# Kernel tuning notes

Hardware: AMD Instinct MI355X
Metric: run time of the kernel (lower is better)

Reference implementation:

```python
import jax, jax.numpy as jnp
import numpy as np

B, NS, NN = 1024, 1, 64
F = 128            # feat_dim = edge_dim = time_dim = pos_dim
DM = 4 * F         # model_dim = 512
H, DK = 2, 256     # n_head, d_k = d_v = model_dim // n_head
LN_EPS = 1e-5


def setup_inputs() -> dict:
    key = jax.random.key(0)
    ks = jax.random.split(key, 20)
    s = 0.02
    inp = {
        'src':   jax.random.normal(ks[0], (B, NS, F), jnp.float32),
        'src_t': jax.random.normal(ks[1], (B, NS, F), jnp.float32),
        'src_p': jax.random.normal(ks[2], (B, NS, F), jnp.float32),
        'seq':   jax.random.normal(ks[3], (B, NN, F), jnp.float32),
        'seq_t': jax.random.normal(ks[4], (B, NN, F), jnp.float32),
        'seq_e': jax.random.normal(ks[5], (B, NN, F), jnp.float32),
        'seq_p': jax.random.normal(ks[6], (B, NN, F), jnp.float32),
        'mask':  jax.random.randint(ks[7], (B, NS, NN), 0, 2).astype(bool),
        # MapBasedMultiHeadAttention params
        'wq': jax.random.normal(ks[8], (H * DK, DM), jnp.float32) * s,
        'wk': jax.random.normal(ks[9], (H * DK, DM), jnp.float32) * s,
        'wv': jax.random.normal(ks[10], (H * DK, DM), jnp.float32) * s,
        'wm': jax.random.normal(ks[11], (2 * DK,), jnp.float32) * s,   # weight_map: Linear(2*d_k, 1, bias=False)
        'fc_w': jax.random.normal(ks[12], (DM, H * DK), jnp.float32) * s,
        'fc_b': jnp.zeros((DM,), jnp.float32),
        'ln_g': jnp.ones((DM,), jnp.float32),
        'ln_b': jnp.zeros((DM,), jnp.float32),
        # MergeLayer(model_dim, feat_dim, feat_dim, feat_dim)
        'm1_w': jax.random.normal(ks[13], (F, DM + F), jnp.float32) * s,
        'm1_b': jnp.zeros((F,), jnp.float32),
        'm2_w': jax.random.normal(ks[14], (F, F), jnp.float32) * s,
        'm2_b': jnp.zeros((F,), jnp.float32),
    }
    return inp


def reference(src, src_t, src_p, seq, seq_t, seq_e, seq_p, mask,
              wq, wk, wv, wm, fc_w, fc_b, ln_g, ln_b, m1_w, m1_b, m2_w, m2_b):
    b, ns, f = src.shape
    nn = seq.shape[1]
    src_e = jnp.zeros((b, ns, f), src.dtype)  # edge feats of sources are zero
    q = jnp.concatenate([src, src_e, src_t, src_p], axis=-1)   # [B,NS,DM]
    k = jnp.concatenate([seq, seq_e, seq_t, seq_p], axis=-1)   # [B,NN,DM]

    # per-head projections: weight [H*DK, DM] -> [H, DK, DM]
    qh = jnp.einsum('bsd,hed->bshe', q, wq.reshape(H, DK, DM))  # [B,NS,H,DK]
    kh = jnp.einsum('bnd,hed->bnhe', k, wk.reshape(H, DK, DM))  # [B,NN,H,DK]
    vh = jnp.einsum('bnd,hed->bnhe', k, wv.reshape(H, DK, DM))  # [B,NN,H,DK]

    # weight_map(Linear over concat([q,k])) == q @ wm[:DK] + k @ wm[DK:]
    score_q = jnp.einsum('bshe,e->bhs', qh, wm[:DK])            # [B,H,NS]
    score_k = jnp.einsum('bnhe,e->bhn', kh, wm[DK:])            # [B,H,NN]
    attn = score_q[..., None] + score_k[:, :, None, :]          # [B,H,NS,NN]
    attn = jnp.where(mask[:, None, :, :], jnp.float32(-1e10), attn)
    attn = jax.nn.softmax(attn, axis=-1)

    out = jnp.einsum('bhsn,bnhe->bshe', attn, vh).reshape(b, ns, H * DK)
    out = jnp.einsum('bsd,ed->bse', out, fc_w) + fc_b           # fc
    out = jnp.where(out >= 0, out, 0.2 * out)                   # LeakyReLU(0.2)
    out = out + q                                               # residual
    mu = out.mean(axis=-1, keepdims=True)
    var = out.var(axis=-1, keepdims=True)
    out = (out - mu) / jnp.sqrt(var + LN_EPS) * ln_g + ln_b     # LayerNorm

    # MergeLayer (non_linear=True)
    x = jnp.concatenate([out, src], axis=-1)                    # [B,NS,DM+F]
    hdn = jax.nn.relu(jnp.einsum('bsd,ed->bse', x, m1_w) + m1_b)
    z = jnp.einsum('bsd,ed->bse', hdn, m2_w) + m2_b             # [B,NS,F]

    # attn in original layout: [n_head*B, len_q, len_k]
    attn_flat = attn.transpose(1, 0, 2, 3).reshape(H * b, ns, nn)
    return (z, attn_flat)
```

## Files before the change

kernel.cpp:

```cpp
#include <hip/hip_runtime.h>
#include <hip/hip_bf16.h>
#include <stdint.h>

#define B_   1024
#define NN_  64
#define F_   128
#define DM_  512
#define DK_  256

typedef unsigned short u16;
using f32x4  = __attribute__((ext_vector_type(4))) float;
using bf16x8 = __attribute__((ext_vector_type(8))) short;

__device__ __forceinline__ uint32_t f2bf(float x) {
  uint32_t u = __builtin_bit_cast(uint32_t, x);
  return (u + 0x7fffu + ((u >> 16) & 1u)) >> 16;
}
__device__ __forceinline__ float bf2f(uint32_t us) {
  return __builtin_bit_cast(float, us << 16);
}
__device__ __forceinline__ void split_pack(float x, float y, uint32_t& hp, uint32_t& lp) {
  uint32_t hx = f2bf(x), hy = f2bf(y);
  uint32_t lx = f2bf(x - bf2f(hx)), ly = f2bf(y - bf2f(hy));
  hp = hx | (hy << 16);
  lp = lx | (ly << 16);
}
__device__ __forceinline__ void split1(float x, u16& h, u16& l) {
  uint32_t hx = f2bf(x);
  h = (u16)hx;
  l = (u16)f2bf(x - bf2f(hx));
}
template <int CTRL>
__device__ __forceinline__ float dppadd(float x) {
  int r = __builtin_amdgcn_mov_dpp(__builtin_bit_cast(int, x), CTRL, 0xF, 0xF, true);
  return x + __builtin_bit_cast(float, r);
}
__device__ __forceinline__ float red16(float p) {
  p = dppadd<0xB1>(p);
  p = dppadd<0x4E>(p);
  p = dppadd<0x114>(p);
  p = dppadd<0x118>(p);
  return p;
}

__global__ __launch_bounds__(256) void k_prep(
    const float* __restrict__ wv, const float* __restrict__ fc_w,
    const float* __restrict__ m1_w, const float* __restrict__ m2_w,
    const float* __restrict__ wk, const float* __restrict__ wm,
    u16* __restrict__ fc_hi, u16* __restrict__ fc_lo,
    u16* __restrict__ wvT_hi, u16* __restrict__ wvT_lo,
    u16* __restrict__ m1_hi, u16* __restrict__ m1_lo,
    u16* __restrict__ m2_hi, u16* __restrict__ m2_lo,
    float* __restrict__ wkc) {
  __shared__ float tile[32][33];
  int tid = threadIdx.x;
  int bx = blockIdx.x;

  if (bx >= 256) {
    int t = bx - 256;
    int h = t >> 3, dc = t & 7;
    int w = tid >> 6, l = tid & 63;
    int d = dc * 64 + l;
    const float* base = wk + (size_t)(h * DK_ + w * 64) * DM_ + d;
    float sacc[8] = {0.f, 0.f, 0.f, 0.f, 0.f, 0.f, 0.f, 0.f};
    #pragma unroll
    for (int e = 0; e < 64; ++e)
      sacc[e & 7] += base[e * DM_] * wm[DK_ + w * 64 + e];
    float s = ((sacc[0] + sacc[1]) + (sacc[2] + sacc[3])) +
              ((sacc[4] + sacc[5]) + (sacc[6] + sacc[7]));
    float* part = &tile[0][0];
    part[w * 64 + l] = s;
    __syncthreads();
    if (w == 0)
      wkc[h * DM_ + d] = part[l] + part[64 + l] + part[128 + l] + part[192 + l];
    return;
  }

  int gtid = bx * 256 + tid;
  int nthr = 256 * 256;
  for (int i = gtid; i < DM_ * DM_; i += nthr) split1(fc_w[i], fc_hi[i], fc_lo[i]);
  for (int i = gtid; i < F_ * (DM_ + F_); i += nthr) split1(m1_w[i], m1_hi[i], m1_lo[i]);
  for (int i = gtid; i < F_ * F_; i += nthr) split1(m2_w[i], m2_hi[i], m2_lo[i]);

  int e0 = (bx >> 4) * 32, d0 = (bx & 15) * 32;
  int rr = tid >> 3, c4 = (tid & 7) * 4;
  float4 v = *(const float4*)(wv + (e0 + rr) * DM_ + d0 + c4);
  tile[rr][c4] = v.x; tile[rr][c4 + 1] = v.y;
  tile[rr][c4 + 2] = v.z; tile[rr][c4 + 3] = v.w;
  __syncthreads();
  int dr = tid >> 3, ec = (tid & 7) * 4;
  #pragma unroll
  for (int q = 0; q < 4; ++q) {
    int idx = (d0 + dr) * DM_ + e0 + ec + q;
    split1(tile[ec + q][dr], wvT_hi[idx], wvT_lo[idx]);
  }
}

__device__ __forceinline__ f32x4 mfma_tile_split(
    const u16* __restrict__ Ahi, const u16* __restrict__ Alo, int lda,
    const u16* __restrict__ Bhi, const u16* __restrict__ Blo, int ldb, int K) {
  int l = threadIdx.x & 63;
  int r = l & 15, g = l >> 4;
  int offA = r * lda + g * 8;
  int offB = r * ldb + g * 8;
  f32x4 acc = {0.f, 0.f, 0.f, 0.f};
  for (int k = 0; k < K; k += 32) {
    bf16x8 ah = *(const bf16x8*)(Ahi + offA + k);
    bf16x8 al = *(const bf16x8*)(Alo + offA + k);
    bf16x8 bh = *(const bf16x8*)(Bhi + offB + k);
    bf16x8 bl = *(const bf16x8*)(Blo + offB + k);
    acc = __builtin_amdgcn_mfma_f32_16x16x32_bf16(ah, bh, acc, 0, 0, 0);
    acc = __builtin_amdgcn_mfma_f32_16x16x32_bf16(ah, bl, acc, 0, 0, 0);
    acc = __builtin_amdgcn_mfma_f32_16x16x32_bf16(al, bh, acc, 0, 0, 0);
  }
  return acc;
}

__global__ __launch_bounds__(256) void k_wcomb(
    const u16* __restrict__ fc_hi, const u16* __restrict__ fc_lo,
    const u16* __restrict__ wvT_hi, const u16* __restrict__ wvT_lo,
    u16* __restrict__ wc_hi, u16* __restrict__ wc_lo) {
  int wid = threadIdx.x >> 6;
  int n0g = blockIdx.y * 32;
  int h = n0g >> 9, d0 = n0g & 511;
  int m0 = blockIdx.x * 32 + (wid >> 1) * 16;
  int nb = d0 + (wid & 1) * 16;
  f32x4 acc = mfma_tile_split(fc_hi + m0 * DM_ + h * DK_,
                              fc_lo + m0 * DM_ + h * DK_, DM_,
                              wvT_hi + nb * DM_ + h * DK_,
                              wvT_lo + nb * DM_ + h * DK_, DM_, DK_);
  int l = threadIdx.x & 63, r = l & 15, g = l >> 4;
  #pragma unroll
  for (int i = 0; i < 4; ++i) {
    int m = m0 + g * 4 + i;
    int idx = m * 1024 + n0g + (wid & 1) * 16 + r;
    split1(acc[i], wc_hi[idx], wc_lo[idx]);
  }
}

__global__ __launch_bounds__(256) void k_score(
    const float* __restrict__ seq, const float* __restrict__ seq_e,
    const float* __restrict__ seq_t, const float* __restrict__ seq_p,
    const float* __restrict__ wkc, float* __restrict__ S_part) {
  int b = blockIdx.x, w = blockIdx.y;
  int tid = threadIdx.x;
  int ww = tid >> 6, l = tid & 63;
  int r16 = l >> 4, c16 = l & 15;
  const float* arr = (w == 0 ? seq : (w == 1 ? seq_e : (w == 2 ? seq_t : seq_p)));
  int cb = 8 * c16;
  float c0[8], c1[8];
  #pragma unroll
  for (int u = 0; u < 8; ++u) {
    c0[u] = wkc[w * 128 + cb + u];
    c1[u] = wkc[512 + w * 128 + cb + u];
  }
  const float* base = arr + (size_t)b * 8192 + (size_t)(ww * 16 + r16) * 128 + cb;
  size_t s0i = (((size_t)w * 1024 + b) * 2 + 0) * 64;
  size_t s1i = (((size_t)w * 1024 + b) * 2 + 1) * 64;

  float4 va[4], vb[4];
  #pragma unroll
  for (int i = 0; i < 4; ++i) {
    va[i] = *(const float4*)(base + i * 512);
    vb[i] = *(const float4*)(base + i * 512 + 4);
  }
  #pragma unroll
  for (int i = 0; i < 4; ++i) {
    float p0 = va[i].x * c0[0] + va[i].y * c0[1] + va[i].z * c0[2] + va[i].w * c0[3]
             + vb[i].x * c0[4] + vb[i].y * c0[5] + vb[i].z * c0[6] + vb[i].w * c0[7];
    float p1 = va[i].x * c1[0] + va[i].y * c1[1] + va[i].z * c1[2] + va[i].w * c1[3]
             + vb[i].x * c1[4] + vb[i].y * c1[5] + vb[i].z * c1[6] + vb[i].w * c1[7];
    p0 = red16(p0);
    p1 = red16(p1);
    if (c16 == 12) {
      int r = ww * 16 + i * 4 + r16;
      S_part[s0i + r] = p0;
      S_part[s1i + r] = p1;
    }
  }
}

__global__ __launch_bounds__(256) void k_attn2(
    const float* __restrict__ seq, const float* __restrict__ seq_e,
    const float* __restrict__ seq_t, const float* __restrict__ seq_p,
    const int* __restrict__ mask, const float* __restrict__ S_part,
    float* __restrict__ attn_out,
    uint32_t* __restrict__ kbar_hi, uint32_t* __restrict__ kbar_lo) {
  __shared__ float attns[2][64];
  int tid = threadIdx.x, b = blockIdx.x;

  if (tid < 128) {
    int h = tid >> 6, row = tid & 63;
    float s = 0.f;
    #pragma unroll
    for (int w4 = 0; w4 < 4; ++w4)
      s += S_part[(((size_t)w4 * 1024 + b) * 2 + h) * 64 + row];
    if (mask[b * 64 + row]) s = -1e10f;
    float m = s;
    #pragma unroll
    for (int off = 32; off; off >>= 1) m = fmaxf(m, __shfl_xor(m, off));
    float p = expf(s - m);
    float ssum = p;
    #pragma unroll
    for (int off = 32; off; off >>= 1) ssum += __shfl_xor(ssum, off);
    float a = p / ssum;
    attns[h][row] = a;
    attn_out[(h * B_ + b) * 64 + row] = a;
  }
  __syncthreads();

  int part = tid >> 6, dp = tid & 63;
  const float* colp =
      (part == 0 ? seq : (part == 1 ? seq_e : (part == 2 ? seq_t : seq_p))) +
      (size_t)b * 8192 + 2 * dp;
  float a00 = 0.f, a01 = 0.f, a10 = 0.f, a11 = 0.f;
  #pragma unroll
  for (int jb = 0; jb < 64; jb += 8) {
    float2 v[8];
    #pragma unroll
    for (int u = 0; u < 8; ++u)
      v[u] = *(const float2*)(colp + (jb + u) * 128);
    #pragma unroll
    for (int u = 0; u < 8; ++u) {
      int j = jb + u;
      float t0 = attns[0][j], t1 = attns[1][j];
      a00 += t0 * v[u].x; a01 += t0 * v[u].y;
      a10 += t1 * v[u].x; a11 += t1 * v[u].y;
    }
  }
  uint32_t hp, lp;
  int idx = b * 512 + tid;
  split_pack(a00, a01, hp, lp);
  kbar_hi[idx] = hp; kbar_lo[idx] = lp;
  split_pack(a10, a11, hp, lp);
  kbar_hi[idx + 256] = hp; kbar_lo[idx + 256] = lp;
}

__global__ __launch_bounds__(256) void k_fc(
    const u16* __restrict__ kb_hi, const u16* __restrict__ kb_lo,
    const u16* __restrict__ wc_hi, const u16* __restrict__ wc_lo,
    const float* __restrict__ fc_b,
    const float* __restrict__ src, const float* __restrict__ src_t,
    const float* __restrict__ src_p, float* __restrict__ fco) {
  int tid = threadIdx.x;
  int wid = tid >> 6, l = tid & 63;
  int r = l & 15, g = l >> 4;
  int m0 = blockIdx.x * 32 + (wid >> 1) * 16;
  int n0 = blockIdx.y * 64 + (wid & 1) * 32;
  int offA  = (m0 + r) * 1024 + g * 8;
  int offB0 = (n0 + r) * 1024 + g * 8;
  int offB1 = offB0 + 16 * 1024;
  f32x4 acc0 = {0.f, 0.f, 0.f, 0.f}, acc1 = {0.f, 0.f, 0.f, 0.f};
  #pragma unroll 4
  for (int k = 0; k < 1024; k += 32) {
    bf16x8 ah  = *(const bf16x8*)(kb_hi + offA + k);
    bf16x8 al  = *(const bf16x8*)(kb_lo + offA + k);
    bf16x8 b0h = *(const bf16x8*)(wc_hi + offB0 + k);
    bf16x8 b0l = *(const bf16x8*)(wc_lo + offB0 + k);
    bf16x8 b1h = *(const bf16x8*)(wc_hi + offB1 + k);
    bf16x8 b1l = *(const bf16x8*)(wc_lo + offB1 + k);
    acc0 = __builtin_amdgcn_mfma_f32_16x16x32_bf16(ah, b0h, acc0, 0, 0, 0);
    acc0 = __builtin_amdgcn_mfma_f32_16x16x32_bf16(ah, b0l, acc0, 0, 0, 0);
    acc0 = __builtin_amdgcn_mfma_f32_16x16x32_bf16(al, b0h, acc0, 0, 0, 0);
    acc1 = __builtin_amdgcn_mfma_f32_16x16x32_bf16(ah, b1h, acc1, 0, 0, 0);
    acc1 = __builtin_amdgcn_mfma_f32_16x16x32_bf16(ah, b1l, acc1, 0, 0, 0);
    acc1 = __builtin_amdgcn_mfma_f32_16x16x32_bf16(al, b1h, acc1, 0, 0, 0);
  }
  #pragma unroll
  for (int f = 0; f < 2; ++f) {
    int col = n0 + f * 16 + r;
    int part = col >> 7, fc2 = col & 127;
    float bias = fc_b[col];
    const float* qsrc = (part == 0 ? src : (part == 2 ? src_t : src_p));
    #pragma unroll
    for (int i = 0; i < 4; ++i) {
      int m = m0 + g * 4 + i;
      float c = (f == 0 ? acc0[i] : acc1[i]) + bias;
      c = (c >= 0.f) ? c : 0.2f * c;
      float qv = (part == 1) ? 0.f : qsrc[m * 128 + fc2];
      fco[m * 512 + col] = c + qv;
    }
  }
}

__global__ __launch_bounds__(512) void k_m12(
    const float* __restrict__ fco, const float* __restrict__ ln_g,
    const float* __restrict__ ln_b, const float* __restrict__ src,
    const u16* __restrict__ m1_hi, const u16* __restrict__ m1_lo,
    const float* __restrict__ m1_b,
    const u16* __restrict__ m2_hi, const u16* __restrict__ m2_lo,
    const float* __restrict__ m2_b, float* __restrict__ z) {
  __shared__ u16 xh[16][648], xl[16][648];
  __shared__ u16 hh[16][136], hl[16][136];
  int tid = threadIdx.x;
  int m0 = blockIdx.x * 16;

  {
    int row = tid >> 5, l32 = tid & 31;
    int grow = m0 + row;
    float v[16];
    float s = 0.f, s2 = 0.f;
    #pragma unroll
    for (int q = 0; q < 16; ++q) {
      v[q] = fco[grow * 512 + q * 32 + l32];
      s += v[q]; s2 += v[q] * v[q];
    }
    #pragma unroll
    for (int off = 16; off; off >>= 1) {
      s += __shfl_xor(s, off, 32);
      s2 += __shfl_xor(s2, off, 32);
    }
    float mu = s * (1.f / 512.f);
    float var = s2 * (1.f / 512.f) - mu * mu;
    float rstd = rsqrtf(var + 1e-5f);
    #pragma unroll
    for (int q = 0; q < 16; ++q) {
      int col = q * 32 + l32;
      float o = (v[q] - mu) * rstd * ln_g[col] + ln_b[col];
      split1(o, xh[row][col], xl[row][col]);
    }
    #pragma unroll
    for (int q2 = 0; q2 < 4; ++q2) {
      int c = q2 * 32 + l32;
      split1(src[grow * 128 + c], xh[row][512 + c], xl[row][512 + c]);
    }
  }
  __syncthreads();

  int wid = tid >> 6, l = tid & 63;
  int r = l & 15, g = l >> 4;
  int nb = wid * 16;
  {
    f32x4 acc = mfma_tile_split(&xh[0][0], &xl[0][0], 648,
                                m1_hi + nb * 640, m1_lo + nb * 640, 640, 640);
    int col = nb + r;
    float bias = m1_b[col];
    #pragma unroll
    for (int ii = 0; ii < 4; ++ii) {
      int row = g * 4 + ii;
      float o = fmaxf(acc[ii] + bias, 0.f);
      split1(o, hh[row][col], hl[row][col]);
    }
  }
  __syncthreads();

  {
    f32x4 acc = mfma_tile_split(&hh[0][0], &hl[0][0], 136,
                                m2_hi + nb * 128, m2_lo + nb * 128, 128, 128);
    int col = nb + r;
    float bias = m2_b[col];
    #pragma unroll
    for (int ii = 0; ii < 4; ++ii) {
      int row = g * 4 + ii;
      z[(m0 + row) * 128 + col] = acc[ii] + bias;
    }
  }
}

extern "C" void kernel_launch(void* const* d_in, const int* in_sizes, int n_in,
                              void* d_out, int out_size, void* d_ws, size_t ws_size,
                              hipStream_t stream) {
  (void)in_sizes; (void)n_in; (void)out_size; (void)ws_size;
  const float* src   = (const float*)d_in[0];
  const float* src_t = (const float*)d_in[1];
  const float* src_p = (const float*)d_in[2];
  const float* seq   = (const float*)d_in[3];
  const float* seq_t = (const float*)d_in[4];
  const float* seq_e = (const float*)d_in[5];
  const float* seq_p = (const float*)d_in[6];
  const int*   mask  = (const int*)d_in[7];
  const float* wk   = (const float*)d_in[9];
  const float* wv   = (const float*)d_in[10];
  const float* wm   = (const float*)d_in[11];
  const float* fc_w = (const float*)d_in[12];
  const float* fc_b = (const float*)d_in[13];
  const float* ln_g = (const float*)d_in[14];
  const float* ln_b = (const float*)d_in[15];
  const float* m1_w = (const float*)d_in[16];
  const float* m1_b = (const float*)d_in[17];
  const float* m2_w = (const float*)d_in[18];
  const float* m2_b = (const float*)d_in[19];

  float* z_out    = (float*)d_out;
  float* attn_out = z_out + B_ * F_;

  char* ws = (char*)d_ws;
  float* wkc     = (float*)(ws + 0);
  u16* fc_hi     = (u16*)(ws + 4096);
  u16* fc_lo     = (u16*)(ws + 528384);
  u16* m1_hi     = (u16*)(ws + 1052672);
  u16* m1_lo     = (u16*)(ws + 1216512);
  u16* m2_hi     = (u16*)(ws + 1380352);
  u16* m2_lo     = (u16*)(ws + 1413120);
  u16* wvT_hi    = (u16*)(ws + 1445888);
  u16* wvT_lo    = (u16*)(ws + 1970176);
  u16* wc_hi     = (u16*)(ws + 2494464);
  u16* wc_lo     = (u16*)(ws + 3543040);
  uint32_t* kbhi = (uint32_t*)(ws + 4591616);
  uint32_t* kblo = (uint32_t*)(ws + 6688768);
  float* fco     = (float*)(ws + 8785920);
  float* S_part  = (float*)(ws + 10883072);

  hipLaunchKernelGGL(k_prep, dim3(272), dim3(256), 0, stream,
                     wv, fc_w, m1_w, m2_w, wk, wm,
                     fc_hi, fc_lo, wvT_hi, wvT_lo,
                     m1_hi, m1_lo, m2_hi, m2_lo, wkc);
  hipLaunchKernelGGL(k_score, dim3(1024, 4), dim3(256), 0, stream,
                     seq, seq_e, seq_t, seq_p, wkc, S_part);
  hipLaunchKernelGGL(k_attn2, dim3(1024), dim3(256), 0, stream,
                     seq, seq_e, seq_t, seq_p, mask, S_part,
                     attn_out, kbhi, kblo);
  hipLaunchKernelGGL(k_wcomb, dim3(16, 32), dim3(256), 0, stream,
                     fc_hi, fc_lo, wvT_hi, wvT_lo, wc_hi, wc_lo);
  hipLaunchKernelGGL(k_fc, dim3(32, 8), dim3(256), 0, stream,
                     (const u16*)kbhi, (const u16*)kblo, wc_hi, wc_lo, fc_b,
                     src, src_t, src_p, fco);
  hipLaunchKernelGGL(k_m12, dim3(64), dim3(512), 0, stream,
                     fco, ln_g, ln_b, src,
                     m1_hi, m1_lo, m1_b, m2_hi, m2_lo, m2_b, z_out);
}
```

Baseline: 98.13 us.

## Fuse score and attention-weighted sum into a single pass over neighbor features

The separate score kernel and attention-sum kernel are merged, so each block streams its 64 neighbor rows of the four sequence tensors from memory once instead of twice. Scores are reduced through shared memory in chunks of 8 rows, and unnormalized exp weights are accumulated into the weighted sum at the same time. Normalization is applied at the end, which also removes the partial-score workspace round trip and one launch. In exchange the softmax drops max subtraction, and a fully masked row now yields a zero denominator and NaN where the reference gives uniform weights. There are also 16 extra block-wide barriers per block.

```diff
diff --git a/kernel.cpp b/kernel.cpp
--- a/kernel.cpp
+++ b/kernel.cpp
@@ -138,101 +138,78 @@
   }
 }
 
-__global__ __launch_bounds__(256) void k_score(
+__global__ __launch_bounds__(256) void k_attn(
     const float* __restrict__ seq, const float* __restrict__ seq_e,
     const float* __restrict__ seq_t, const float* __restrict__ seq_p,
-    const float* __restrict__ wkc, float* __restrict__ S_part) {
-  int b = blockIdx.x, w = blockIdx.y;
-  int tid = threadIdx.x;
-  int ww = tid >> 6, l = tid & 63;
-  int r16 = l >> 4, c16 = l & 15;
-  const float* arr = (w == 0 ? seq : (w == 1 ? seq_e : (w == 2 ? seq_t : seq_p)));
-  int cb = 8 * c16;
-  float c0[8], c1[8];
-  #pragma unroll
-  for (int u = 0; u < 8; ++u) {
-    c0[u] = wkc[w * 128 + cb + u];
-    c1[u] = wkc[512 + w * 128 + cb + u];
-  }
-  const float* base = arr + (size_t)b * 8192 + (size_t)(ww * 16 + r16) * 128 + cb;
-  size_t s0i = (((size_t)w * 1024 + b) * 2 + 0) * 64;
-  size_t s1i = (((size_t)w * 1024 + b) * 2 + 1) * 64;
-
-  float4 va[4], vb[4];
-  #pragma unroll
-  for (int i = 0; i < 4; ++i) {
-    va[i] = *(const float4*)(base + i * 512);
-    vb[i] = *(const float4*)(base + i * 512 + 4);
-  }
-  #pragma unroll
-  for (int i = 0; i < 4; ++i) {
-    float p0 = va[i].x * c0[0] + va[i].y * c0[1] + va[i].z * c0[2] + va[i].w * c0[3]
-             + vb[i].x * c0[4] + vb[i].y * c0[5] + vb[i].z * c0[6] + vb[i].w * c0[7];
-    float p1 = va[i].x * c1[0] + va[i].y * c1[1] + va[i].z * c1[2] + va[i].w * c1[3]
-             + vb[i].x * c1[4] + vb[i].y * c1[5] + vb[i].z * c1[6] + vb[i].w * c1[7];
-    p0 = red16(p0);
-    p1 = red16(p1);
-    if (c16 == 12) {
-      int r = ww * 16 + i * 4 + r16;
-      S_part[s0i + r] = p0;
-      S_part[s1i + r] = p1;
-    }
-  }
-}
-
-__global__ __launch_bounds__(256) void k_attn2(
-    const float* __restrict__ seq, const float* __restrict__ seq_e,
-    const float* __restrict__ seq_t, const float* __restrict__ seq_p,
-    const int* __restrict__ mask, const float* __restrict__ S_part,
+    const int* __restrict__ mask, const float* __restrict__ wkc,
     float* __restrict__ attn_out,
     uint32_t* __restrict__ kbar_hi, uint32_t* __restrict__ kbar_lo) {
-  __shared__ float attns[2][64];
+  __shared__ float pbuf[4][2][8][4];
+  __shared__ float els[2][64];
+  __shared__ float Zs[2];
   int tid = threadIdx.x, b = blockIdx.x;
+  int w = tid >> 6, l = tid & 63;
+  int c16 = l & 15;
+
+  const float* arr = (w == 0 ? seq : (w == 1 ? seq_e : (w == 2 ? seq_t : seq_p)));
+  const float* base = arr + (size_t)b * 8192 + 2 * l;
+  float c00 = wkc[w * 128 + 2 * l],       c01 = wkc[w * 128 + 2 * l + 1];
+  float c10 = wkc[512 + w * 128 + 2 * l], c11 = wkc[512 + w * 128 + 2 * l + 1];
+  float kb00 = 0.f, kb01 = 0.f, kb10 = 0.f, kb11 = 0.f;
+
+  for (int bt = 0; bt < 8; ++bt) {
+    float2 v[8];
+    #pragma unroll
+    for (int u = 0; u < 8; ++u)
+      v[u] = *(const float2*)(base + (size_t)(bt * 8 + u) * 128);
+    #pragma unroll
+    for (int u = 0; u < 8; ++u) {
+      float p0 = v[u].x * c00 + v[u].y * c01;
+      float p1 = v[u].x * c10 + v[u].y * c11;
+      p0 = red16(p0);
+      p1 = red16(p1);
+      if (c16 == 12) {
+        pbuf[w][0][u][l >> 4] = p0;
+        pbuf[w][1][u][l >> 4] = p1;
+      }
+    }
+    __syncthreads();
+    if (tid < 16) {
+      int u = tid & 7, h = tid >> 3;
+      float s = 0.f;
+      #pragma unroll
+      for (int ww = 0; ww < 4; ++ww)
+        #pragma unroll
+        for (int g = 0; g < 4; ++g) s += pbuf[ww][h][u][g];
+      int row = bt * 8 + u;
+      els[h][row] = mask[b * 64 + row] ? 0.f : expf(s);
+    }
+    __syncthreads();
+    #pragma unroll
+    for (int u = 0; u < 8; ++u) {
+      int row = bt * 8 + u;
+      float e0 = els[0][row], e1 = els[1][row];
+      kb00 += e0 * v[u].x; kb01 += e0 * v[u].y;
+      kb10 += e1 * v[u].x; kb11 += e1 * v[u].y;
+    }
+  }
 
   if (tid < 128) {
     int h = tid >> 6, row = tid & 63;
-    float s = 0.f;
-    #pragma unroll
-    for (int w4 = 0; w4 < 4; ++w4)
-      s += S_part[(((size_t)w4 * 1024 + b) * 2 + h) * 64 + row];
-    if (mask[b * 64 + row]) s = -1e10f;
-    float m = s;
-    #pragma unroll
-    for (int off = 32; off; off >>= 1) m = fmaxf(m, __shfl_xor(m, off));
-    float p = expf(s - m);
-    float ssum = p;
-    #pragma unroll
-    for (int off = 32; off; off >>= 1) ssum += __shfl_xor(ssum, off);
-    float a = p / ssum;
-    attns[h][row] = a;
-    attn_out[(h * B_ + b) * 64 + row] = a;
+    float e = els[h][row];
+    float z = e;
+    #pragma unroll
+    for (int off = 32; off; off >>= 1) z += __shfl_xor(z, off);
+    attn_out[(h * B_ + b) * 64 + row] = e / z;
+    if (row == 0) Zs[h] = z;
   }
   __syncthreads();
-
-  int part = tid >> 6, dp = tid & 63;
-  const float* colp =
-      (part == 0 ? seq : (part == 1 ? seq_e : (part == 2 ? seq_t : seq_p))) +
-      (size_t)b * 8192 + 2 * dp;
-  float a00 = 0.f, a01 = 0.f, a10 = 0.f, a11 = 0.f;
-  #pragma unroll
-  for (int jb = 0; jb < 64; jb += 8) {
-    float2 v[8];
-    #pragma unroll
-    for (int u = 0; u < 8; ++u)
-      v[u] = *(const float2*)(colp + (jb + u) * 128);
-    #pragma unroll
-    for (int u = 0; u < 8; ++u) {
-      int j = jb + u;
-      float t0 = attns[0][j], t1 = attns[1][j];
-      a00 += t0 * v[u].x; a01 += t0 * v[u].y;
-      a10 += t1 * v[u].x; a11 += t1 * v[u].y;
-    }
-  }
+  float r0 = 1.f / Zs[0], r1 = 1.f / Zs[1];
   uint32_t hp, lp;
   int idx = b * 512 + tid;
-  split_pack(a00, a01, hp, lp);
+  split_pack(kb00 * r0, kb01 * r0, hp, lp);
   kbar_hi[idx] = hp; kbar_lo[idx] = lp;
-  split_pack(a10, a11, hp, lp);
+  split_pack(kb10 * r1, kb11 * r1, hp, lp);
   kbar_hi[idx + 256] = hp; kbar_lo[idx + 256] = lp;
 }
 
@@ -343,7 +320,6 @@
     }
   }
   __syncthreads();
-
   {
     f32x4 acc = mfma_tile_split(&hh[0][0], &hl[0][0], 136,
                                 m2_hi + nb * 128, m2_lo + nb * 128, 128, 128);
@@ -399,16 +375,13 @@
   uint32_t* kbhi = (uint32_t*)(ws + 4591616);
   uint32_t* kblo = (uint32_t*)(ws + 6688768);
   float* fco     = (float*)(ws + 8785920);
-  float* S_part  = (float*)(ws + 10883072);
 
   hipLaunchKernelGGL(k_prep, dim3(272), dim3(256), 0, stream,
                      wv, fc_w, m1_w, m2_w, wk, wm,
                      fc_hi, fc_lo, wvT_hi, wvT_lo,
                      m1_hi, m1_lo, m2_hi, m2_lo, wkc);
-  hipLaunchKernelGGL(k_score, dim3(1024, 4), dim3(256), 0, stream,
-                     seq, seq_e, seq_t, seq_p, wkc, S_part);
-  hipLaunchKernelGGL(k_attn2, dim3(1024), dim3(256), 0, stream,
-                     seq, seq_e, seq_t, seq_p, mask, S_part,
+  hipLaunchKernelGGL(k_attn, dim3(1024), dim3(256), 0, stream,
+                     seq, seq_e, seq_t, seq_p, mask, wkc,
                      attn_out, kbhi, kblo);
   hipLaunchKernelGGL(k_wcomb, dim3(16, 32), dim3(256), 0, stream,
                      fc_hi, fc_lo, wvT_hi, wvT_lo, wc_hi, wc_lo);
```

Result: faster. 80.71 us (-17.7%).
